# Performance work log

Hardware: AMD Instinct MI355X
Metric: run time of the kernel (lower is better)

## Reference

```python
import jax, jax.numpy as jnp
import numpy as np

H = 16  # n_heads

def _split_heads(x, n_heads):
    B, S, Dm = x.shape
    return x.reshape(B, S, n_heads, Dm // n_heads).transpose(0, 2, 1, 3)  # [B,H,S,D]

def _matmul_prefix_sum(x, y, z):
    """Faithful, efficient form of the TF matmul_prefix_sum.
    TF builds yz[s] = y[s] (x) z[s] outer products, cumsums over s, then
    contracts with x[t]/ (t+1).  That equals a causal-masked bilinear form:
      out[t, j] = (1/(t+1)) * sum_{s<=t} (x[t]. y[s]) * z[s, j]
    so we compute (x y^T * tril / idx) @ z without the 5D intermediate.
    """
    S = x.shape[2]
    idx = jnp.arange(1, S + 1, dtype=x.dtype)[:, None]        # position 1..S
    mask = jnp.tril(jnp.ones((S, S), dtype=x.dtype))
    scores = jnp.einsum('bhtd,bhsd->bhts', x, y) * (mask / idx)
    return jnp.einsum('bhts,bhsj->bhtj', scores, z)

def setup_inputs() -> dict:
    key = jax.random.key(0)
    ks = jax.random.split(key, 12)
    B, S, Dm = 2, 1024, 1024
    f32 = jnp.float32
    rn = lambda k, shp: jax.random.normal(k, shp, dtype=f32)
    w_scale = f32(1.0 / np.sqrt(Dm))
    return {
        'v': rn(ks[0], (B, S, Dm)),
        'k': rn(ks[1], (B, S, Dm)),
        'q': rn(ks[2], (B, S, Dm)),
        'p': rn(ks[3], (B, S, Dm)),
        'wq_k': rn(ks[4], (Dm, Dm)) * w_scale, 'wq_b': jnp.zeros((Dm,), f32),
        'wk_k': rn(ks[5], (Dm, Dm)) * w_scale, 'wk_b': jnp.zeros((Dm,), f32),
        'wv_k': rn(ks[6], (Dm, Dm)) * w_scale, 'wv_b': jnp.zeros((Dm,), f32),
        'wc_k': rn(ks[7], (Dm, Dm)) * w_scale, 'wc_b': jnp.zeros((Dm,), f32),
    }

def reference(v, k, q, p, wq_k, wq_b, wk_k, wk_b, wv_k, wv_b, wc_k, wc_b):
    B, S, Dm = q.shape
    D = Dm // H
    norm_d = 1.0 / jnp.sqrt(jnp.asarray(D, q.dtype))
    ph = _split_heads(p, H)                                    # [B,H,S,D]
    qh = _split_heads((q @ wq_k + wq_b) * norm_d, H)
    kh = _split_heads(k @ wk_k + wk_b, H)
    vh = _split_heads(v @ wv_k + wv_b, H)
    # elu(p q^T)+1 then transpose -> indexed [B,H,t(query),s(p-position)]
    attn_pack = jax.nn.elu(jnp.einsum('bhtd,bhsd->bhts', qh, ph)) + 1.0
    attn_unpack = _matmul_prefix_sum(qh, kh, attn_pack)        # [B,H,S,S]
    attn_unpack = jax.nn.softmax(attn_unpack, axis=-1)
    attn_out = _matmul_prefix_sum(attn_unpack, attn_pack, vh)  # [B,H,S,D]
    attn_out = attn_out.transpose(0, 2, 1, 3).reshape(B, S, Dm)
    return attn_out @ wc_k + wc_b
```

## Files before the change

### kernel.cpp

```cpp
#include <hip/hip_runtime.h>

#define DEVI static __device__ __forceinline__

using s16x8 = __attribute__((ext_vector_type(8))) short;
using f32x4 = __attribute__((ext_vector_type(4))) float;
using u32x4 = __attribute__((ext_vector_type(4))) unsigned int;

static constexpr int H  = 16;
static constexpr int S  = 1024;
static constexpr int DM = 1024;
static constexpr int NB = 2;
static constexpr int BS = NB * S;
static constexpr long SS  = (long)S * S;
static constexpr long HSS = (long)H * SS;
static constexpr long SDM = (long)S * DM;

DEVI unsigned short f2bf(float f) {
    union { float f; unsigned u; } c; c.f = f;
    c.u += 0x7FFFu + ((c.u >> 16) & 1u);
    return (unsigned short)(c.u >> 16);
}
DEVI float bf2f(unsigned short v) {
    union { unsigned u; float f; } c; c.u = ((unsigned)v) << 16;
    return c.f;
}

DEVI void gload16(const unsigned short* g, unsigned short* l) {
    __builtin_amdgcn_global_load_lds(
        (const __attribute__((address_space(1))) unsigned int*)g,
        (__attribute__((address_space(3))) unsigned int*)l, 16, 0, 0);
}

enum { EPI_BFB = 0, EPI_VTB, EPI_PACK, EPI_PACK2, EPI_MASK, EPI_BF, EPI_OUT };

template<int EPI, bool CK, bool CS, bool SWZ, bool REVY>
__global__ __launch_bounds__(256)
void gemmS(const unsigned short* __restrict__ Aall, long a_sb, long a_sh, int lda,
           const unsigned short* __restrict__ Ball, long b_sb, long b_sh, int ldb,
           void* __restrict__ Oall, void* __restrict__ O2, long o_sb, long o_sh, int ldo,
           const float* __restrict__ bias, int bstride, int K, int NV)
{
    int bx, by, bz;
    if (SWZ) {
        const int L = (int)blockIdx.x + ((int)blockIdx.y << 3) + ((int)blockIdx.z << 6);
        const int g = L & 7, r = L >> 3;
        bz = g + ((r >> 6) << 3);
        bx = r & 7;
        by = 7 - ((r >> 3) & 7);
    } else {
        bx = blockIdx.x;
        by = REVY ? (int)gridDim.y - 1 - (int)blockIdx.y : (int)blockIdx.y;
        bz = blockIdx.z;
    }
    const int m0 = by * 128, n0 = bx * 128;
    if (CS && n0 > m0 + 127) return;
    const int zb = bz >> 4, zh = bz & 15;
    const unsigned short* Ap = Aall + (long)zb * a_sb + (long)zh * a_sh;
    const unsigned short* Bp = Ball + (long)zb * b_sb + (long)zh * b_sh;
    const float* bi = bias + (long)zh * bstride;

    __shared__ alignas(16) unsigned short lA[128 * 64];
    __shared__ alignas(16) unsigned short lB[128 * 64];

    const int tid = threadIdx.x, w = tid >> 6, lane = tid & 63;
    const int lr = lane & 15, lg = lane >> 4;
    const int wm = (w >> 1) << 6, wn = (w & 1) << 6;

    const unsigned short* gA[4]; const unsigned short* gB[4]; int lo[4];
#pragma unroll
    for (int i = 0; i < 4; ++i) {
        const int q = (i * 4 + w) * 64 + lane, row = q >> 3, slot = q & 7;
        const int gs = (slot ^ (row & 7)) * 8;
        gA[i] = Ap + (long)(m0 + row) * lda + gs;
        int rb = n0 + row; if (rb >= NV) rb = NV - 1;
        gB[i] = Bp + (long)rb * ldb + gs;
        lo[i] = (i * 4 + w) * 512;
    }

    int abase[4], axor[4], bbase[4], bxor[4];
#pragma unroll
    for (int f = 0; f < 4; ++f) {
        const int ra = wm + f * 16 + lr;
        abase[f] = ra * 64; axor[f] = (ra & 7) * 8;
        const int rb = wn + f * 16 + lr;
        bbase[f] = rb * 64; bxor[f] = (rb & 7) * 8;
    }

    f32x4 acc[4][4] = {};
    const int Keff = CK ? ((K < m0 + 128) ? K : m0 + 128) : K;

    for (int k0 = 0; k0 < Keff; k0 += 64) {
#pragma unroll
        for (int i = 0; i < 4; ++i) {
            gload16(gA[i] + k0, &lA[lo[i]]);
            gload16(gB[i] + k0, &lB[lo[i]]);
        }
        __syncthreads();
#pragma unroll
        for (int kk = 0; kk < 64; kk += 32) {
            s16x8 af[4], bv[4];
#pragma unroll
            for (int f = 0; f < 4; ++f) {
                af[f] = *reinterpret_cast<const s16x8*>(&lA[abase[f] + ((kk + 8 * lg) ^ axor[f])]);
                bv[f] = *reinterpret_cast<const s16x8*>(&lB[bbase[f] + ((kk + 8 * lg) ^ bxor[f])]);
            }
#pragma unroll
            for (int fm = 0; fm < 4; ++fm)
#pragma unroll
                for (int fn = 0; fn < 4; ++fn)
                    acc[fm][fn] = __builtin_amdgcn_mfma_f32_16x16x32_bf16(af[fm], bv[fn], acc[fm][fn], 0, 0, 0);
        }
        __syncthreads();
    }

    const long obase = (long)zb * o_sb + (long)zh * o_sh;
#pragma unroll
    for (int fm = 0; fm < 4; ++fm)
#pragma unroll
        for (int fn = 0; fn < 4; ++fn) {
            const int t0 = m0 + wm + fm * 16 + lg * 4;
            const int gn = n0 + wn + fn * 16 + lr;
            if (gn >= NV) continue;
            if constexpr (EPI == EPI_PACK2) {
                ushort4 pt;
                unsigned short* o1 = (unsigned short*)Oall;
                unsigned short* o2 = (unsigned short*)O2;
#pragma unroll
                for (int r = 0; r < 4; ++r) {
                    float vv = acc[fm][fn][r];
                    vv = vv > 0.f ? vv + 1.f : __expf(vv);
                    const unsigned short b = f2bf(vv);
                    o1[obase + (long)(t0 + r) * ldo + gn] = b;
                    ((unsigned short*)&pt)[r] = b;
                }
                *reinterpret_cast<ushort4*>(&o2[obase + (long)gn * ldo + t0]) = pt;
            } else {
#pragma unroll
                for (int r = 0; r < 4; ++r) {
                    const int gm = t0 + r;
                    float vv = acc[fm][fn][r];
                    const long o = obase + (long)gm * ldo + gn;
                    if constexpr (EPI == EPI_BFB) {
                        ((unsigned short*)Oall)[o] = f2bf(vv + bi[gn]);
                    } else if constexpr (EPI == EPI_VTB) {
                        ((unsigned short*)Oall)[o] = f2bf(vv + bi[gm]);
                    } else if constexpr (EPI == EPI_PACK) {
                        vv = vv > 0.f ? vv + 1.f : __expf(vv);
                        ((unsigned short*)Oall)[o] = f2bf(vv);
                    } else if constexpr (EPI == EPI_MASK) {
                        vv = (gn <= gm) ? vv / (float)(gm + 1) : 0.f;
                        ((unsigned short*)Oall)[o] = f2bf(vv);
                    } else if constexpr (EPI == EPI_BF) {
                        ((unsigned short*)Oall)[o] = f2bf(vv);
                    } else {
                        ((float*)Oall)[o] = vv + bi[gn];
                    }
                }
            }
        }
}

__global__ __launch_bounds__(256)
void softmax_rows(const unsigned short* __restrict__ in, unsigned short* __restrict__ out)
{
    const int w = threadIdx.x >> 6, lane = threadIdx.x & 63;
    const long row = (long)blockIdx.x * 4 + w;
    const u32x4* r4 = reinterpret_cast<const u32x4*>(in + row * S);
    u32x4 a = r4[lane * 2], b = r4[lane * 2 + 1];
    float v[16];
#pragma unroll
    for (int i = 0; i < 4; ++i) {
        v[2*i]     = bf2f((unsigned short)(a[i] & 0xFFFF));
        v[2*i+1]   = bf2f((unsigned short)(a[i] >> 16));
        v[8+2*i]   = bf2f((unsigned short)(b[i] & 0xFFFF));
        v[8+2*i+1] = bf2f((unsigned short)(b[i] >> 16));
    }
    float mx = v[0];
#pragma unroll
    for (int i = 1; i < 16; ++i) mx = fmaxf(mx, v[i]);
#pragma unroll
    for (int off = 32; off; off >>= 1) mx = fmaxf(mx, __shfl_xor(mx, off));
    float e[16], s = 0.f;
#pragma unroll
    for (int i = 0; i < 16; ++i) { e[i] = __expf(v[i] - mx); s += e[i]; }
#pragma unroll
    for (int off = 32; off; off >>= 1) s += __shfl_xor(s, off);
    const float inv = 1.f / s;
    u32x4 oa, ob;
#pragma unroll
    for (int i = 0; i < 4; ++i) {
        oa[i] = (unsigned)f2bf(e[2*i]   * inv) | ((unsigned)f2bf(e[2*i+1]   * inv) << 16);
        ob[i] = (unsigned)f2bf(e[8+2*i] * inv) | ((unsigned)f2bf(e[8+2*i+1] * inv) << 16);
    }
    u32x4* o4 = reinterpret_cast<u32x4*>(out + row * S);
    o4[lane * 2] = oa; o4[lane * 2 + 1] = ob;
}

__global__ __launch_bounds__(256)
void cast4(const float* __restrict__ s0, const float* __restrict__ s1,
           const float* __restrict__ s2, const float* __restrict__ s3,
           unsigned short* __restrict__ dst, int n4)
{
    const int i = blockIdx.x * 256 + threadIdx.x;
    if (i >= n4) return;
    const float* s = (blockIdx.z == 0) ? s0 : (blockIdx.z == 1) ? s1 : (blockIdx.z == 2) ? s2 : s3;
    float4 x = reinterpret_cast<const float4*>(s)[i];
    ushort4 o; o.x = f2bf(x.x); o.y = f2bf(x.y); o.z = f2bf(x.z); o.w = f2bf(x.w);
    reinterpret_cast<ushort4*>(dst + (size_t)blockIdx.z * n4 * 4)[i] = o;
}

__global__ __launch_bounds__(256)
void twcast4(const float* __restrict__ s0, const float* __restrict__ s1,
             const float* __restrict__ s2, const float* __restrict__ s3,
             unsigned short* __restrict__ dstall, int n)
{
    __shared__ unsigned short t[64][72];
    const float* src = (blockIdx.z == 0) ? s0 : (blockIdx.z == 1) ? s1 : (blockIdx.z == 2) ? s2 : s3;
    const float scale = (blockIdx.z == 0) ? 0.125f : 1.0f;
    unsigned short* dst = dstall + (size_t)blockIdx.z * n * n;
    const int r0 = blockIdx.y * 64, c0 = blockIdx.x * 64;
    const int lrow = threadIdx.x >> 2, lseg = (threadIdx.x & 3) << 4;
    const float4* g4 = reinterpret_cast<const float4*>(src + (long)(r0 + lrow) * n + c0 + lseg);
    alignas(16) unsigned short tmp[16];
#pragma unroll
    for (int q = 0; q < 4; ++q) {
        float4 x = g4[q];
        tmp[4*q+0] = f2bf(x.x * scale); tmp[4*q+1] = f2bf(x.y * scale);
        tmp[4*q+2] = f2bf(x.z * scale); tmp[4*q+3] = f2bf(x.w * scale);
    }
#pragma unroll
    for (int j = 0; j < 16; ++j) t[lrow][lseg + j] = tmp[j];
    __syncthreads();
#pragma unroll
    for (int j = 0; j < 16; ++j) tmp[j] = t[lseg + j][lrow];
    unsigned short* d = dst + (long)(c0 + lrow) * n + r0 + lseg;
    *reinterpret_cast<u32x4*>(d)     = *reinterpret_cast<const u32x4*>(tmp);
    *reinterpret_cast<u32x4*>(d + 8) = *reinterpret_cast<const u32x4*>(tmp + 8);
}

__global__ __launch_bounds__(256)
void bias2(const float* __restrict__ a, const float* __restrict__ b, float* __restrict__ dst)
{
    const int i = blockIdx.x * 256 + threadIdx.x;
    if (i < DM) { dst[i] = a[i] * 0.125f; dst[DM + i] = b[i]; }
}

extern "C" void kernel_launch(void* const* d_in, const int* in_sizes, int n_in,
                              void* d_out, int out_size, void* d_ws, size_t ws_size,
                              hipStream_t stream)
{
    (void)in_sizes; (void)n_in; (void)out_size;
    const float* v_in = (const float*)d_in[0];
    const float* k_in = (const float*)d_in[1];
    const float* q_in = (const float*)d_in[2];
    const float* p_in = (const float*)d_in[3];
    const float* wq   = (const float*)d_in[4];
    const float* wqb  = (const float*)d_in[5];
    const float* wk   = (const float*)d_in[6];
    const float* wkb  = (const float*)d_in[7];
    const float* wvw  = (const float*)d_in[8];
    const float* wvb  = (const float*)d_in[9];
    const float* wc   = (const float*)d_in[10];
    const float* wcb  = (const float*)d_in[11];
    float* out = (float*)d_out;

    char* ws = (char*)d_ws;
    size_t off = 0;
    auto take = [&](size_t n) { char* p = ws + off; off += (n + 255) & ~(size_t)255; return p; };
    unsigned short* qbf = (unsigned short*)take((size_t)BS * DM * 2);
    unsigned short* kbf = (unsigned short*)take((size_t)BS * DM * 2);
    unsigned short* vbf = (unsigned short*)take((size_t)BS * DM * 2);
    unsigned short* pbf = (unsigned short*)take((size_t)BS * DM * 2);
    unsigned short* wqT = (unsigned short*)take((size_t)DM * DM * 2);
    unsigned short* wkT = (unsigned short*)take((size_t)DM * DM * 2);
    unsigned short* wvT = (unsigned short*)take((size_t)DM * DM * 2);
    unsigned short* wcT = (unsigned short*)take((size_t)DM * DM * 2);
    float*          bq2 = (float*)take((size_t)2 * DM * 4);
    unsigned short* qh  = (unsigned short*)take((size_t)BS * DM * 2);
    unsigned short* kh  = (unsigned short*)take((size_t)BS * DM * 2);
    unsigned short* vhT = (unsigned short*)take((size_t)BS * DM * 2);
    unsigned short* ao  = (unsigned short*)take((size_t)BS * DM * 2);
    const size_t ssz = (size_t)NB * HSS * 2;
    unsigned short* B1 = (unsigned short*)take(ssz);
    unsigned short* B2 = (unsigned short*)take(ssz);
    unsigned short* B3 = (unsigned short*)take(ssz);
    const bool dual = (ws_size >= off + ssz);
    unsigned short* B4 = dual ? (unsigned short*)take(ssz) : nullptr;
    (void)kbf; (void)wkT;

    const int n4 = BS * DM / 4;
    const dim3 blk(256);

    cast4<<<dim3(n4 / 256, 1, 4), blk, 0, stream>>>(q_in, k_in, v_in, p_in, qbf, n4);
    twcast4<<<dim3(16, 16, 4), blk, 0, stream>>>(wq, wk, wvw, wc, wqT, DM);
    bias2<<<dim3(4), blk, 0, stream>>>(wqb, wkb, bq2);

    gemmS<EPI_BFB,false,false,false,false><<<dim3(8, 16, 2), blk, 0, stream>>>(
        qbf, 0, (long)BS*DM, DM,  wqT, 0, (long)DM*DM, DM,  qh, nullptr, 0, (long)BS*DM, DM,
        bq2, DM, DM, DM);
    gemmS<EPI_VTB,false,false,false,false><<<dim3(8, 8, 2), blk, 0, stream>>>(
        wvT, 0, 0, DM,  vbf, 0, SDM, DM,  vhT, nullptr, 0, (long)DM*S, S,
        wvb, 0, DM, S);

    unsigned short *sqkbuf, *ptbuf, *pbuf = B1, *lbuf;
    if (dual) {
        gemmS<EPI_PACK2,false,false,true,false><<<dim3(8, 8, 32), blk, 0, stream>>>(
            qh, SDM, 64, DM,  pbf, SDM, 64, DM,  B1, B2, HSS, SS, S,  wvb, 0, 64, S);
        ptbuf = B2; sqkbuf = B3; lbuf = B4;
    } else {
        gemmS<EPI_PACK,false,false,true,false><<<dim3(8, 8, 32), blk, 0, stream>>>(
            pbf, SDM, 64, DM,  qh, SDM, 64, DM,  B1, nullptr, HSS, SS, S,  wvb, 0, 64, S);
        ptbuf = B1; sqkbuf = B2; lbuf = B3;
    }
    gemmS<EPI_MASK,false,true,true,false><<<dim3(8, 8, 32), blk, 0, stream>>>(
        qh, SDM, 64, DM,  kh, SDM, 64, DM,  sqkbuf, nullptr, HSS, SS, S,  wvb, 0, 64, S);
    gemmS<EPI_BF,true,false,true,false><<<dim3(8, 8, 32), blk, 0, stream>>>(
        sqkbuf, HSS, SS, S,  ptbuf, HSS, SS, S,  lbuf, nullptr, HSS, SS, S,  wvb, 0, S, S);
    softmax_rows<<<dim3(NB*H*S/4), blk, 0, stream>>>(lbuf, sqkbuf);
    if (!dual) {
        gemmS<EPI_PACK,false,false,true,false><<<dim3(8, 8, 32), blk, 0, stream>>>(
            qh, SDM, 64, DM,  pbf, SDM, 64, DM,  B1, nullptr, HSS, SS, S,  wvb, 0, 64, S);
    }
    gemmS<EPI_MASK,false,true,true,false><<<dim3(8, 8, 32), blk, 0, stream>>>(
        sqkbuf, HSS, SS, S,  pbuf, HSS, SS, S,  lbuf, nullptr, HSS, SS, S,  wvb, 0, S, S);
    gemmS<EPI_BF,true,false,false,true><<<dim3(1, 8, 32), blk, 0, stream>>>(
        lbuf, HSS, SS, S,  vhT, (long)DM*S, (long)64*S, S,  ao, nullptr, SDM, 64, DM,
        wvb, 0, S, 64);
    gemmS<EPI_OUT,false,false,false,false><<<dim3(8, 16, 1), blk, 0, stream>>>(
        ao, 0, 0, DM,  wcT, 0, 0, DM,  out, nullptr, 0, 0, DM,  wcb, 0, DM, DM);
}
```

Measured before the change: 308.7 us.

## Add 256x256-tile 8-wave GEMM kernel for the two large S×S×S batched products

Introduces a new gemm8 kernel with 256x256 output tiles, 512 threads, double-buffered LDS loaded by direct global-to-LDS copies, and phased MFMA quads using setprio and barriers. It replaces the generic gemmS for the two heavy S×S×S products (the causal-K EPI_BF and the causally-masked EPI_MASK). Larger tiles raise arithmetic intensity and cut global traffic, and staggering the loads across phases overlaps memory with MFMA work. The cost is 128 KB of LDS per block, giving one block per CU, and heavy register use from 32 accumulators per thread.

```diff
diff --git a/kernel.cpp b/kernel.cpp
--- a/kernel.cpp
+++ b/kernel.cpp
@@ -32,6 +32,127 @@
 }
 
 enum { EPI_BFB = 0, EPI_VTB, EPI_PACK, EPI_PACK2, EPI_MASK, EPI_BF, EPI_OUT };
+
+template<int EPI, bool CK, bool CS>
+__global__ __launch_bounds__(512)
+void gemm8(const unsigned short* __restrict__ Aall,
+           const unsigned short* __restrict__ Ball,
+           unsigned short* __restrict__ Oall, int K)
+{
+    const int L   = (int)blockIdx.x + ((int)blockIdx.y << 2) + ((int)blockIdx.z << 4);
+    const int xcd = L & 7, idx = L >> 3;
+    const int bz  = xcd + ((idx >> 4) << 3);
+    const int by  = 3 - ((idx >> 2) & 3);
+    const int bx  = idx & 3;
+    const int m0 = by * 256, n0 = bx * 256;
+    if (CS && n0 > m0 + 255) return;
+    const unsigned short* Ap = Aall + (long)bz * SS;
+    const unsigned short* Bp = Ball + (long)bz * SS;
+
+    __shared__ alignas(16) unsigned short lds[65536];
+
+    const int tid = threadIdx.x, w = tid >> 6, lane = tid & 63;
+    const int lr = lane & 15, lg = lane >> 4;
+    const int wm = w >> 2, wn = w & 3;
+
+    const unsigned short* gA[4]; const unsigned short* gB[4]; int lo[4];
+#pragma unroll
+    for (int i = 0; i < 4; ++i) {
+        const int c = i * 512 + w * 64 + lane, row = c >> 3, slot = c & 7;
+        const int gs = (slot ^ (row & 7)) * 8;
+        gA[i] = Ap + (long)(m0 + row) * S + gs;
+        gB[i] = Bp + (long)(n0 + row) * S + gs;
+        lo[i] = (i * 512 + w * 64) * 8;
+    }
+
+    f32x4 acc[8][4] = {};
+    const int Keff = CK ? ((K < m0 + 256) ? K : m0 + 256) : K;
+    const int nt = Keff >> 6;
+
+#define STAGE_A(T, B) do { const long ko_ = (long)(T) << 6;                    \
+    gload16(gA[0] + ko_, lds + (B) * 16384 + lo[0]);                           \
+    gload16(gA[1] + ko_, lds + (B) * 16384 + lo[1]);                           \
+    gload16(gA[2] + ko_, lds + (B) * 16384 + lo[2]);                           \
+    gload16(gA[3] + ko_, lds + (B) * 16384 + lo[3]); } while (0)
+#define STAGE_B(T, B) do { const long ko_ = (long)(T) << 6;                    \
+    gload16(gB[0] + ko_, lds + 32768 + (B) * 16384 + lo[0]);                   \
+    gload16(gB[1] + ko_, lds + 32768 + (B) * 16384 + lo[1]);                   \
+    gload16(gB[2] + ko_, lds + 32768 + (B) * 16384 + lo[2]);                   \
+    gload16(gB[3] + ko_, lds + 32768 + (B) * 16384 + lo[3]); } while (0)
+
+#define QUAD(R2, C2) do {                                                      \
+    s16x8 qa[4][2], qb[2][2];                                                  \
+    _Pragma("unroll") for (int f = 0; f < 4; ++f) {                            \
+        const int ra = wm * 128 + (R2) * 64 + f * 16 + lr;                     \
+        const int rx = (ra & 7) * 8;                                           \
+        qa[f][0] = *reinterpret_cast<const s16x8*>(&lAb[ra * 64 + ((8 * lg) ^ rx)]);        \
+        qa[f][1] = *reinterpret_cast<const s16x8*>(&lAb[ra * 64 + ((32 + 8 * lg) ^ rx)]);   \
+    }                                                                          \
+    _Pragma("unroll") for (int f = 0; f < 2; ++f) {                            \
+        const int rb = wn * 64 + (C2) * 32 + f * 16 + lr;                      \
+        const int rx = (rb & 7) * 8;                                           \
+        qb[f][0] = *reinterpret_cast<const s16x8*>(&lBb[rb * 64 + ((8 * lg) ^ rx)]);        \
+        qb[f][1] = *reinterpret_cast<const s16x8*>(&lBb[rb * 64 + ((32 + 8 * lg) ^ rx)]);   \
+    }                                                                          \
+    __builtin_amdgcn_s_setprio(1);                                             \
+    _Pragma("unroll") for (int f = 0; f < 4; ++f)                              \
+        _Pragma("unroll") for (int g = 0; g < 2; ++g) {                        \
+            acc[(R2)*4+f][(C2)*2+g] = __builtin_amdgcn_mfma_f32_16x16x32_bf16( \
+                qa[f][0], qb[g][0], acc[(R2)*4+f][(C2)*2+g], 0, 0, 0);         \
+            acc[(R2)*4+f][(C2)*2+g] = __builtin_amdgcn_mfma_f32_16x16x32_bf16( \
+                qa[f][1], qb[g][1], acc[(R2)*4+f][(C2)*2+g], 0, 0, 0);         \
+        }                                                                      \
+    __builtin_amdgcn_s_setprio(0);                                             \
+} while (0)
+
+#define PHASE_END do { __builtin_amdgcn_sched_barrier(0);                      \
+    __builtin_amdgcn_s_barrier();                                              \
+    __builtin_amdgcn_sched_barrier(0); } while (0)
+
+    STAGE_A(0, 0); STAGE_B(0, 0);
+
+    for (int t = 0; t < nt; ++t) {
+        const int b = t & 1;
+        const unsigned short* lAb = lds + b * 16384;
+        const unsigned short* lBb = lds + 32768 + b * 16384;
+        asm volatile("s_waitcnt vmcnt(0)" ::: "memory");
+        __builtin_amdgcn_s_barrier();
+        __builtin_amdgcn_sched_barrier(0);
+        if (t + 1 < nt) STAGE_A(t + 1, b ^ 1);
+        QUAD(0, 0);
+        PHASE_END;
+        if (t + 1 < nt) STAGE_B(t + 1, b ^ 1);
+        QUAD(0, 1);
+        PHASE_END;
+        QUAD(1, 0);
+        PHASE_END;
+        QUAD(1, 1);
+        __builtin_amdgcn_sched_barrier(0);
+    }
+#undef STAGE_A
+#undef STAGE_B
+#undef QUAD
+#undef PHASE_END
+
+    const long obase = (long)bz * SS;
+#pragma unroll
+    for (int fm = 0; fm < 8; ++fm)
+#pragma unroll
+        for (int fn = 0; fn < 4; ++fn)
+#pragma unroll
+            for (int r = 0; r < 4; ++r) {
+                const int gm = m0 + wm * 128 + fm * 16 + lg * 4 + r;
+                const int gn = n0 + wn * 64 + fn * 16 + lr;
+                float vv = acc[fm][fn][r];
+                const long o = obase + (long)gm * S + gn;
+                if constexpr (EPI == EPI_MASK) {
+                    vv = (gn <= gm) ? vv / (float)(gm + 1) : 0.f;
+                    Oall[o] = f2bf(vv);
+                } else {
+                    Oall[o] = f2bf(vv);
+                }
+            }
+}
 
 template<int EPI, bool CK, bool CS, bool SWZ, bool REVY>
 __global__ __launch_bounds__(256)
@@ -314,15 +435,15 @@
     }
     gemmS<EPI_MASK,false,true,true,false><<<dim3(8, 8, 32), blk, 0, stream>>>(
         qh, SDM, 64, DM,  kh, SDM, 64, DM,  sqkbuf, nullptr, HSS, SS, S,  wvb, 0, 64, S);
-    gemmS<EPI_BF,true,false,true,false><<<dim3(8, 8, 32), blk, 0, stream>>>(
-        sqkbuf, HSS, SS, S,  ptbuf, HSS, SS, S,  lbuf, nullptr, HSS, SS, S,  wvb, 0, S, S);
+    gemm8<EPI_BF,true,false><<<dim3(4, 4, 32), dim3(512), 0, stream>>>(
+        sqkbuf, ptbuf, lbuf, S);
     softmax_rows<<<dim3(NB*H*S/4), blk, 0, stream>>>(lbuf, sqkbuf);
     if (!dual) {
         gemmS<EPI_PACK,false,false,true,false><<<dim3(8, 8, 32), blk, 0, stream>>>(
             qh, SDM, 64, DM,  pbf, SDM, 64, DM,  B1, nullptr, HSS, SS, S,  wvb, 0, 64, S);
     }
-    gemmS<EPI_MASK,false,true,true,false><<<dim3(8, 8, 32), blk, 0, stream>>>(
-        sqkbuf, HSS, SS, S,  pbuf, HSS, SS, S,  lbuf, nullptr, HSS, SS, S,  wvb, 0, S, S);
+    gemm8<EPI_MASK,false,true><<<dim3(4, 4, 32), dim3(512), 0, stream>>>(
+        sqkbuf, pbuf, lbuf, S);
     gemmS<EPI_BF,true,false,false,true><<<dim3(1, 8, 32), blk, 0, stream>>>(
         lbuf, HSS, SS, S,  vhT, (long)DM*S, (long)64*S, S,  ao, nullptr, SDM, 64, DM,
         wvb, 0, S, 64);
```

Result: slower. 334.5 us (+8.4%).

## Fold softmax exp into GEMM epilogue and template tile sizes per GEMM

Applied to the files above, without the earlier changes.

The softmax is split up. Exponentials are computed in the epilogue of the score GEMM without subtracting the row max. A light kernel then computes only the reciprocal row sums, and the normalization is folded into the next masked GEMM's epilogue as a per-row scale. This removes a full read-modify-write pass over the large score tensor. Separately, the GEMM kernel is templated on tile shape so the projection GEMMs and the narrow attention-output GEMM use smaller tiles, giving more blocks and less padded work. Skipping the max subtraction risks exp overflow if scores grow large.

```diff
diff --git a/kernel.cpp b/kernel.cpp
--- a/kernel.cpp
+++ b/kernel.cpp
@@ -31,15 +31,18 @@
         (__attribute__((address_space(3))) unsigned int*)l, 16, 0, 0);
 }
 
-enum { EPI_BFB = 0, EPI_VTB, EPI_PACK, EPI_PACK2, EPI_MASK, EPI_BF, EPI_OUT };
-
-template<int EPI, bool CK, bool CS, bool SWZ, bool REVY>
-__global__ __launch_bounds__(256)
-void gemmS(const unsigned short* __restrict__ Aall, long a_sb, long a_sh, int lda,
+enum { EPI_BFB = 0, EPI_VTB, EPI_PACK, EPI_PACK2, EPI_MASK, EPI_EXP, EPI_SMASK, EPI_BF, EPI_OUT };
+
+template<int TM, int TN, int EPI, bool CK, bool CS, bool SWZ, bool REVY>
+__global__ __launch_bounds__((TM/64)*(TN/64)*64)
+void gemmT(const unsigned short* __restrict__ Aall, long a_sb, long a_sh, int lda,
            const unsigned short* __restrict__ Ball, long b_sb, long b_sh, int ldb,
            void* __restrict__ Oall, void* __restrict__ O2, long o_sb, long o_sh, int ldo,
            const float* __restrict__ bias, int bstride, int K, int NV)
 {
+    constexpr int WN = TN / 64, WM = TM / 64, NWV = WM * WN, NTHR = NWV * 64;
+    constexpr int IA = (TM * 8) / NTHR, IB = (TN * 8) / NTHR;
+
     int bx, by, bz;
     if (SWZ) {
         const int L = (int)blockIdx.x + ((int)blockIdx.y << 3) + ((int)blockIdx.z << 6);
@@ -52,29 +55,34 @@
         by = REVY ? (int)gridDim.y - 1 - (int)blockIdx.y : (int)blockIdx.y;
         bz = blockIdx.z;
     }
-    const int m0 = by * 128, n0 = bx * 128;
-    if (CS && n0 > m0 + 127) return;
+    const int m0 = by * TM, n0 = bx * TN;
+    if (CS && n0 > m0 + TM - 1) return;
     const int zb = bz >> 4, zh = bz & 15;
     const unsigned short* Ap = Aall + (long)zb * a_sb + (long)zh * a_sh;
     const unsigned short* Bp = Ball + (long)zb * b_sb + (long)zh * b_sh;
     const float* bi = bias + (long)zh * bstride;
 
-    __shared__ alignas(16) unsigned short lA[128 * 64];
-    __shared__ alignas(16) unsigned short lB[128 * 64];
+    __shared__ alignas(16) unsigned short lA[TM * 64];
+    __shared__ alignas(16) unsigned short lB[TN * 64];
 
     const int tid = threadIdx.x, w = tid >> 6, lane = tid & 63;
     const int lr = lane & 15, lg = lane >> 4;
-    const int wm = (w >> 1) << 6, wn = (w & 1) << 6;
-
-    const unsigned short* gA[4]; const unsigned short* gB[4]; int lo[4];
-#pragma unroll
-    for (int i = 0; i < 4; ++i) {
-        const int q = (i * 4 + w) * 64 + lane, row = q >> 3, slot = q & 7;
-        const int gs = (slot ^ (row & 7)) * 8;
-        gA[i] = Ap + (long)(m0 + row) * lda + gs;
+    const int wm = (w / WN) * 64, wn = (w % WN) * 64;
+
+    const unsigned short* gA[IA]; int loA[IA];
+    const unsigned short* gB[IB]; int loB[IB];
+#pragma unroll
+    for (int i = 0; i < IA; ++i) {
+        const int q = i * NTHR + tid, row = q >> 3, slot = q & 7;
+        gA[i]  = Ap + (long)(m0 + row) * lda + ((slot ^ (row & 7)) * 8);
+        loA[i] = (i * NWV + w) * 512;
+    }
+#pragma unroll
+    for (int i = 0; i < IB; ++i) {
+        const int q = i * NTHR + tid, row = q >> 3, slot = q & 7;
         int rb = n0 + row; if (rb >= NV) rb = NV - 1;
-        gB[i] = Bp + (long)rb * ldb + gs;
-        lo[i] = (i * 4 + w) * 512;
+        gB[i]  = Bp + (long)rb * ldb + ((slot ^ (row & 7)) * 8);
+        loB[i] = (i * NWV + w) * 512;
     }
 
     int abase[4], axor[4], bbase[4], bxor[4];
@@ -87,14 +95,13 @@
     }
 
     f32x4 acc[4][4] = {};
-    const int Keff = CK ? ((K < m0 + 128) ? K : m0 + 128) : K;
+    const int Keff = CK ? ((K < m0 + TM) ? K : m0 + TM) : K;
 
     for (int k0 = 0; k0 < Keff; k0 += 64) {
 #pragma unroll
-        for (int i = 0; i < 4; ++i) {
-            gload16(gA[i] + k0, &lA[lo[i]]);
-            gload16(gB[i] + k0, &lB[lo[i]]);
-        }
+        for (int i = 0; i < IA; ++i) gload16(gA[i] + k0, &lA[loA[i]]);
+#pragma unroll
+        for (int i = 0; i < IB; ++i) gload16(gB[i] + k0, &lB[loB[i]]);
         __syncthreads();
 #pragma unroll
         for (int kk = 0; kk < 64; kk += 32) {
@@ -150,6 +157,11 @@
                     } else if constexpr (EPI == EPI_MASK) {
                         vv = (gn <= gm) ? vv / (float)(gm + 1) : 0.f;
                         ((unsigned short*)Oall)[o] = f2bf(vv);
+                    } else if constexpr (EPI == EPI_EXP) {
+                        ((unsigned short*)Oall)[o] = f2bf(__expf(vv));
+                    } else if constexpr (EPI == EPI_SMASK) {
+                        vv = (gn <= gm) ? vv * bias[(long)bz * S + gm] / (float)(gm + 1) : 0.f;
+                        ((unsigned short*)Oall)[o] = f2bf(vv);
                     } else if constexpr (EPI == EPI_BF) {
                         ((unsigned short*)Oall)[o] = f2bf(vv);
                     } else {
@@ -161,39 +173,21 @@
 }
 
 __global__ __launch_bounds__(256)
-void softmax_rows(const unsigned short* __restrict__ in, unsigned short* __restrict__ out)
+void rowsum_inv(const unsigned short* __restrict__ E, float* __restrict__ inv)
 {
     const int w = threadIdx.x >> 6, lane = threadIdx.x & 63;
     const long row = (long)blockIdx.x * 4 + w;
-    const u32x4* r4 = reinterpret_cast<const u32x4*>(in + row * S);
+    const u32x4* r4 = reinterpret_cast<const u32x4*>(E + row * S);
     u32x4 a = r4[lane * 2], b = r4[lane * 2 + 1];
-    float v[16];
+    float s = 0.f;
 #pragma unroll
     for (int i = 0; i < 4; ++i) {
-        v[2*i]     = bf2f((unsigned short)(a[i] & 0xFFFF));
-        v[2*i+1]   = bf2f((unsigned short)(a[i] >> 16));
-        v[8+2*i]   = bf2f((unsigned short)(b[i] & 0xFFFF));
-        v[8+2*i+1] = bf2f((unsigned short)(b[i] >> 16));
-    }
-    float mx = v[0];
-#pragma unroll
-    for (int i = 1; i < 16; ++i) mx = fmaxf(mx, v[i]);
-#pragma unroll
-    for (int off = 32; off; off >>= 1) mx = fmaxf(mx, __shfl_xor(mx, off));
-    float e[16], s = 0.f;
-#pragma unroll
-    for (int i = 0; i < 16; ++i) { e[i] = __expf(v[i] - mx); s += e[i]; }
+        s += bf2f((unsigned short)(a[i] & 0xFFFF)) + bf2f((unsigned short)(a[i] >> 16));
+        s += bf2f((unsigned short)(b[i] & 0xFFFF)) + bf2f((unsigned short)(b[i] >> 16));
+    }
 #pragma unroll
     for (int off = 32; off; off >>= 1) s += __shfl_xor(s, off);
-    const float inv = 1.f / s;
-    u32x4 oa, ob;
-#pragma unroll
-    for (int i = 0; i < 4; ++i) {
-        oa[i] = (unsigned)f2bf(e[2*i]   * inv) | ((unsigned)f2bf(e[2*i+1]   * inv) << 16);
-        ob[i] = (unsigned)f2bf(e[8+2*i] * inv) | ((unsigned)f2bf(e[8+2*i+1] * inv) << 16);
-    }
-    u32x4* o4 = reinterpret_cast<u32x4*>(out + row * S);
-    o4[lane * 2] = oa; o4[lane * 2 + 1] = ob;
+    if (lane == 0) inv[row] = 1.f / s;
 }
 
 __global__ __launch_bounds__(256)
@@ -276,6 +270,7 @@
     unsigned short* wvT = (unsigned short*)take((size_t)DM * DM * 2);
     unsigned short* wcT = (unsigned short*)take((size_t)DM * DM * 2);
     float*          bq2 = (float*)take((size_t)2 * DM * 4);
+    float*          inv = (float*)take((size_t)NB * H * S * 4);
     unsigned short* qh  = (unsigned short*)take((size_t)BS * DM * 2);
     unsigned short* kh  = (unsigned short*)take((size_t)BS * DM * 2);
     unsigned short* vhT = (unsigned short*)take((size_t)BS * DM * 2);
@@ -289,43 +284,43 @@
     (void)kbf; (void)wkT;
 
     const int n4 = BS * DM / 4;
-    const dim3 blk(256);
-
-    cast4<<<dim3(n4 / 256, 1, 4), blk, 0, stream>>>(q_in, k_in, v_in, p_in, qbf, n4);
-    twcast4<<<dim3(16, 16, 4), blk, 0, stream>>>(wq, wk, wvw, wc, wqT, DM);
-    bias2<<<dim3(4), blk, 0, stream>>>(wqb, wkb, bq2);
-
-    gemmS<EPI_BFB,false,false,false,false><<<dim3(8, 16, 2), blk, 0, stream>>>(
+    const dim3 b256(256), b128(128);
+
+    cast4<<<dim3(n4 / 256, 1, 4), b256, 0, stream>>>(q_in, k_in, v_in, p_in, qbf, n4);
+    twcast4<<<dim3(16, 16, 4), b256, 0, stream>>>(wq, wk, wvw, wc, wqT, DM);
+    bias2<<<dim3(4), b256, 0, stream>>>(wqb, wkb, bq2);
+
+    gemmT<64,128,EPI_BFB,false,false,false,false><<<dim3(8, 32, 2), b128, 0, stream>>>(
         qbf, 0, (long)BS*DM, DM,  wqT, 0, (long)DM*DM, DM,  qh, nullptr, 0, (long)BS*DM, DM,
         bq2, DM, DM, DM);
-    gemmS<EPI_VTB,false,false,false,false><<<dim3(8, 8, 2), blk, 0, stream>>>(
+    gemmT<64,128,EPI_VTB,false,false,false,false><<<dim3(8, 16, 2), b128, 0, stream>>>(
         wvT, 0, 0, DM,  vbf, 0, SDM, DM,  vhT, nullptr, 0, (long)DM*S, S,
         wvb, 0, DM, S);
 
-    unsigned short *sqkbuf, *ptbuf, *pbuf = B1, *lbuf;
+    unsigned short *sqkbuf, *ptbuf, *pbuf, *ebuf, *s2buf;
     if (dual) {
-        gemmS<EPI_PACK2,false,false,true,false><<<dim3(8, 8, 32), blk, 0, stream>>>(
+        gemmT<128,128,EPI_PACK2,false,false,true,false><<<dim3(8, 8, 32), b256, 0, stream>>>(
             qh, SDM, 64, DM,  pbf, SDM, 64, DM,  B1, B2, HSS, SS, S,  wvb, 0, 64, S);
-        ptbuf = B2; sqkbuf = B3; lbuf = B4;
+        pbuf = B1; ptbuf = B2; sqkbuf = B3; ebuf = B4; s2buf = B3;
     } else {
-        gemmS<EPI_PACK,false,false,true,false><<<dim3(8, 8, 32), blk, 0, stream>>>(
+        gemmT<128,128,EPI_PACK,false,false,true,false><<<dim3(8, 8, 32), b256, 0, stream>>>(
             pbf, SDM, 64, DM,  qh, SDM, 64, DM,  B1, nullptr, HSS, SS, S,  wvb, 0, 64, S);
-        ptbuf = B1; sqkbuf = B2; lbuf = B3;
-    }
-    gemmS<EPI_MASK,false,true,true,false><<<dim3(8, 8, 32), blk, 0, stream>>>(
+        ptbuf = B1; sqkbuf = B2; ebuf = B3; pbuf = B1; s2buf = B2;
+    }
+    gemmT<128,128,EPI_MASK,false,true,true,false><<<dim3(8, 8, 32), b256, 0, stream>>>(
         qh, SDM, 64, DM,  kh, SDM, 64, DM,  sqkbuf, nullptr, HSS, SS, S,  wvb, 0, 64, S);
-    gemmS<EPI_BF,true,false,true,false><<<dim3(8, 8, 32), blk, 0, stream>>>(
-        sqkbuf, HSS, SS, S,  ptbuf, HSS, SS, S,  lbuf, nullptr, HSS, SS, S,  wvb, 0, S, S);
-    softmax_rows<<<dim3(NB*H*S/4), blk, 0, stream>>>(lbuf, sqkbuf);
+    gemmT<128,128,EPI_EXP,true,false,true,false><<<dim3(8, 8, 32), b256, 0, stream>>>(
+        sqkbuf, HSS, SS, S,  ptbuf, HSS, SS, S,  ebuf, nullptr, HSS, SS, S,  wvb, 0, S, S);
+    rowsum_inv<<<dim3(NB*H*S/4), b256, 0, stream>>>(ebuf, inv);
     if (!dual) {
-        gemmS<EPI_PACK,false,false,true,false><<<dim3(8, 8, 32), blk, 0, stream>>>(
+        gemmT<128,128,EPI_PACK,false,false,true,false><<<dim3(8, 8, 32), b256, 0, stream>>>(
             qh, SDM, 64, DM,  pbf, SDM, 64, DM,  B1, nullptr, HSS, SS, S,  wvb, 0, 64, S);
     }
-    gemmS<EPI_MASK,false,true,true,false><<<dim3(8, 8, 32), blk, 0, stream>>>(
-        sqkbuf, HSS, SS, S,  pbuf, HSS, SS, S,  lbuf, nullptr, HSS, SS, S,  wvb, 0, S, S);
-    gemmS<EPI_BF,true,false,false,true><<<dim3(1, 8, 32), blk, 0, stream>>>(
-        lbuf, HSS, SS, S,  vhT, (long)DM*S, (long)64*S, S,  ao, nullptr, SDM, 64, DM,
+    gemmT<128,128,EPI_SMASK,false,true,true,false><<<dim3(8, 8, 32), b256, 0, stream>>>(
+        ebuf, HSS, SS, S,  pbuf, HSS, SS, S,  s2buf, nullptr, HSS, SS, S,  inv, 0, S, S);
+    gemmT<128,64,EPI_BF,true,false,false,true><<<dim3(1, 8, 32), b128, 0, stream>>>(
+        s2buf, HSS, SS, S,  vhT, (long)DM*S, (long)64*S, S,  ao, nullptr, SDM, 64, DM,
         wvb, 0, S, 64);
-    gemmS<EPI_OUT,false,false,false,false><<<dim3(8, 16, 1), blk, 0, stream>>>(
+    gemmT<64,128,EPI_OUT,false,false,false,false><<<dim3(8, 32, 1), b128, 0, stream>>>(
         ao, 0, 0, DM,  wcT, 0, 0, DM,  out, nullptr, 0, 0, DM,  wcb, 0, DM, DM);
 }
```

Measured after the change: 307.9 us. Within noise of the previous version (-0.2%).
